# Performance work log

Measured on AMD Instinct MI355X. Metric: run time of the kernel, lower is better.

Reference implementation:

```python
import jax, jax.numpy as jnp
import numpy as np

H = 512          # HIDDEN_DIM
W = 480          # WINDOWWIDTH
NL = 8           # NUMLABELS (output_dim)
STEPS = W // 15  # 32 decoder steps
ATT = W // 16    # 30 attention positions
B = 4            # window batch
L = 12           # per-frame sequence length
D_IN = 32        # input_dim
N = B * W        # 1920 frame sequences


def _lstm(x, Wih, Whh, bih, bhh):
    # x: [T, Bn, Din] -> per-step hidden/cell states [T, Bn, Hd] (torch LSTM gate order i,f,g,o)
    xp = x @ Wih.T + (bih + bhh)
    h0 = jnp.zeros((x.shape[1], Whh.shape[1]), x.dtype)
    def step(carry, xt):
        h, c = carry
        g = xt + h @ Whh.T
        i, f, gg, o = jnp.split(g, 4, axis=-1)
        c = jax.nn.sigmoid(f) * c + jax.nn.sigmoid(i) * jnp.tanh(gg)
        h = jax.nn.sigmoid(o) * jnp.tanh(c)
        return (h, c), (h, c)
    _, (hs, cs) = jax.lax.scan(step, (h0, h0), xp)
    return hs, cs


def _bilstm(x, Wf, Uf, bf, cf, Wb, Ub, bb, cb):
    # x: [Bt, T, D] batch_first; returns ([Bt, T, 2H], h_fwd_final, h_bwd_final)
    xt = jnp.swapaxes(x, 0, 1)
    hf, _ = _lstm(xt, Wf, Uf, bf, cf)
    hb, _ = _lstm(xt[::-1], Wb, Ub, bb, cb)
    out = jnp.concatenate([hf, hb[::-1]], axis=-1)
    return jnp.swapaxes(out, 0, 1), hf[-1], hb[-1]


def _forward(xs, xlengths, enc_Wih, enc_Whh, enc_bih, enc_bhh,
             penc_Wih_f, penc_Whh_f, penc_bih_f, penc_bhh_f,
             penc_Wih_b, penc_Whh_b, penc_bih_b, penc_bhh_b,
             attn_W, attn_b, comb_W, comb_b,
             gru_Wih, gru_Whh, gru_bih, gru_bhh, out_W, out_b):
    # frame-level encoder: packed sequences -> (h, c) at each sequence's true length
    hs, cs = _lstm(xs, enc_Wih, enc_Whh, enc_bih, enc_bhh)   # [L, N, H] each
    idx = xlengths - 1
    ar = jnp.arange(N)
    ctx = jnp.concatenate([hs[idx, ar], cs[idx, ar]], axis=-1)  # [N, 2H]
    ctx = ctx.reshape(B, W // 2, 4 * H)
    # pyramidal BiLSTM stack (dropout is identity at eval)
    out = ctx
    hf = hb = None
    for i in range(4):
        out, hf, hb = _bilstm(ctx, penc_Wih_f[i], penc_Whh_f[i], penc_bih_f[i], penc_bhh_f[i],
                              penc_Wih_b[i], penc_Whh_b[i], penc_bih_b[i], penc_bhh_b[i])
        if i < 3:
            ctx = out.reshape(B, W // (2 ** (i + 2)), 4 * H)
    enc_out = out                                   # [B, ATT, 2H]
    hidden0 = jnp.concatenate([hf, hb], axis=-1)    # [B, 2H]

    def dstep(carry, _):
        inp, h = carry                              # [B, NL], [B, 2H]
        aw = jax.nn.softmax(jnp.concatenate([inp, h], axis=-1) @ attn_W.T + attn_b, axis=-1)
        ctxv = jnp.einsum('bt,btd->bd', aw, enc_out)
        x = jax.nn.relu(jnp.concatenate([inp, ctxv], axis=-1) @ comb_W.T + comb_b)
        # torch GRU cell (gate order r, z, n)
        gi = x @ gru_Wih.T + gru_bih
        gh = h @ gru_Whh.T + gru_bhh
        ir, iz, inn = jnp.split(gi, 3, axis=-1)
        hr, hz, hn = jnp.split(gh, 3, axis=-1)
        r = jax.nn.sigmoid(ir + hr)
        z = jax.nn.sigmoid(iz + hz)
        n = jnp.tanh(inn + r * hn)
        hnew = (1.0 - z) * n + z * h
        logp = jax.nn.log_softmax(hnew @ out_W.T + out_b, axis=-1)
        return (logp, hnew), logp                   # free-running: next input = log-probs

    inp0 = jnp.zeros((B, NL), xs.dtype)
    _, outs = jax.lax.scan(dstep, (inp0, hidden0), None, length=STEPS)  # [STEPS, B, NL]
    return jnp.swapaxes(outs, 0, 1).reshape(B * STEPS, NL)


def setup_inputs() -> dict:
    key = jax.random.key(0)
    ks = jax.random.split(key, 24)
    s = 0.03
    def nrm(k, shape):
        return jax.random.normal(k, shape, dtype=jnp.float32) * s
    return {
        'xs': jax.random.normal(ks[0], (L, N, D_IN), dtype=jnp.float32),
        'xlengths': jax.random.randint(ks[1], (N,), 1, L + 1, dtype=jnp.int32),
        'enc_Wih': nrm(ks[2], (4 * H, D_IN)),
        'enc_Whh': nrm(ks[3], (4 * H, H)),
        'enc_bih': nrm(ks[4], (4 * H,)),
        'enc_bhh': nrm(ks[5], (4 * H,)),
        'penc_Wih_f': nrm(ks[6], (4, 4 * H, 4 * H)),
        'penc_Whh_f': nrm(ks[7], (4, 4 * H, H)),
        'penc_bih_f': nrm(ks[8], (4, 4 * H)),
        'penc_bhh_f': nrm(ks[9], (4, 4 * H)),
        'penc_Wih_b': nrm(ks[10], (4, 4 * H, 4 * H)),
        'penc_Whh_b': nrm(ks[11], (4, 4 * H, H)),
        'penc_bih_b': nrm(ks[12], (4, 4 * H)),
        'penc_bhh_b': nrm(ks[13], (4, 4 * H)),
        'attn_W': nrm(ks[14], (ATT, 2 * H + NL)),
        'attn_b': nrm(ks[15], (ATT,)),
        'comb_W': nrm(ks[16], (H, 2 * H + NL)),
        'comb_b': nrm(ks[17], (H,)),
        'gru_Wih': nrm(ks[18], (3 * 2 * H, H)),
        'gru_Whh': nrm(ks[19], (3 * 2 * H, 2 * H)),
        'gru_bih': nrm(ks[20], (3 * 2 * H,)),
        'gru_bhh': nrm(ks[21], (3 * 2 * H,)),
        'out_W': nrm(ks[22], (NL, 2 * H)),
        'out_b': nrm(ks[23], (NL,)),
    }


def reference(xs, xlengths, enc_Wih, enc_Whh, enc_bih, enc_bhh,
              penc_Wih_f, penc_Whh_f, penc_bih_f, penc_bhh_f,
              penc_Wih_b, penc_Whh_b, penc_bih_b, penc_bhh_b,
              attn_W, attn_b, comb_W, comb_b,
              gru_Wih, gru_Whh, gru_bih, gru_bhh, out_W, out_b):
    return _forward(xs, xlengths, enc_Wih, enc_Whh, enc_bih, enc_bhh,
                    penc_Wih_f, penc_Whh_f, penc_bih_f, penc_bhh_f,
                    penc_Wih_b, penc_Whh_b, penc_bih_b, penc_bhh_b,
                    attn_W, attn_b, comb_W, comb_b,
                    gru_Wih, gru_Whh, gru_bih, gru_bhh, out_W, out_b)
```

## Files before the change

### kernel.cpp

```cpp
#include <hip/hip_runtime.h>
#include <stdint.h>

typedef __attribute__((ext_vector_type(8))) __bf16 bf16x8;
typedef __attribute__((ext_vector_type(4))) float f32x4;
typedef __attribute__((ext_vector_type(4))) unsigned u32x4;

#define DEVI static __device__ __forceinline__
#define SENT 0xFFFFFFFFu

DEVI bf16x8 bzero8(){ bf16x8 r;
#pragma unroll
  for (int i=0;i<8;++i) r[i]=(__bf16)0.0f; return r; }

DEVI bf16x8 ld8(const __bf16* p){ return *(const bf16x8*)p; }
DEVI void st8(__bf16* p, bf16x8 v){ *(bf16x8*)p = v; }

DEVI f32x4 MFMA(bf16x8 a, bf16x8 b, f32x4 c){
  return __builtin_amdgcn_mfma_f32_16x16x32_bf16(a, b, c, 0, 0, 0);
}

DEVI float sigf(float x){ return 1.0f/(1.0f+__expf(-x)); }

DEVI void ast(unsigned* p, unsigned v){ __hip_atomic_store(p, v, __ATOMIC_RELAXED, __HIP_MEMORY_SCOPE_AGENT); }

DEVI unsigned packbf(float a, float b){
  union { __bf16 h[2]; unsigned u; } x; x.h[0]=(__bf16)a; x.h[1]=(__bf16)b; return x.u;
}
DEVI float bflo(unsigned u){ return __builtin_bit_cast(float, u<<16); }
DEVI float bfhi(unsigned u){ return __builtin_bit_cast(float, u & 0xffff0000u); }

DEVI unsigned bad4(u32x4 v){ return (v[0]==SENT)|(v[1]==SENT)|(v[2]==SENT)|(v[3]==SENT); }

DEVI u32x4 ald4(const void* p){
  u32x4 v;
  asm volatile("global_load_dwordx4 %0, %1, off sc0 sc1\n\ts_waitcnt vmcnt(0)"
               : "=&v"(v) : "v"(p) : "memory");
  return v;
}
DEVI u32x4 poll4(const void* p){
  u32x4 v = ald4(p);
  while (bad4(v)){ __builtin_amdgcn_s_sleep(1); v = ald4(p); }
  return v;
}
DEVI void ald4x2(const void* p, u32x4& a, u32x4& b){
  asm volatile("global_load_dwordx4 %0, %2, off sc0 sc1\n\t"
               "global_load_dwordx4 %1, %2, off offset:16 sc0 sc1\n\t"
               "s_waitcnt vmcnt(0)"
               : "=&v"(a), "=&v"(b) : "v"(p) : "memory");
}
DEVI void poll4x2(const void* p, u32x4& a, u32x4& b){
  ald4x2(p, a, b);
  while (bad4(a) | bad4(b)){ __builtin_amdgcn_s_sleep(1); ald4x2(p, a, b); }
}

DEVI void packGroup(const float* W, int Nsrc, int Kreal, int NT, __bf16* dst, long g){
  int kt = (int)(g / (NT*64));
  int rem = (int)(g % (NT*64));
  int nt = rem >> 6, ln = rem & 63;
  int row = nt*16 + (ln & 15);
  int col = kt*32 + ((ln >> 4) << 3);
  bf16x8 v = bzero8();
  if (row < Nsrc){
#pragma unroll
    for (int j=0;j<8;++j){ int c = col + j; if (c < Kreal) v[j] = (__bf16)W[(long)row*Kreal + c]; }
  }
  st8(dst + g*8, v);
}

DEVI void packGroupCat(const float* Wih, const float* Whh, __bf16* dst, long g){
  int kt = (int)(g / (128*64));
  int rem = (int)(g % (128*64));
  int nt = rem >> 6, ln = rem & 63;
  int prow = nt*16 + (ln & 15);
  int src = (prow & 3)*512 + (prow >> 2);
  int col = kt*32 + ((ln >> 4) << 3);
  bf16x8 v;
  if (col < 32){
#pragma unroll
    for (int j=0;j<8;++j) v[j] = (__bf16)Wih[(long)src*32 + col + j];
  } else {
#pragma unroll
    for (int j=0;j<8;++j) v[j] = (__bf16)Whh[(long)src*512 + (col-32) + j];
  }
  st8(dst + g*8, v);
}

__global__ void initK(unsigned* hb){
  int g = blockIdx.x*256 + threadIdx.x;
  if (g < 6144) hb[2048 + g] = SENT;
}

__global__ void packSmallK(const float* __restrict__ xs, const float* __restrict__ eWih,
    const float* __restrict__ eWhh, const float* __restrict__ ebih, const float* __restrict__ ebhh,
    const float* __restrict__ attnW,
    __bf16* __restrict__ xsb, __bf16* __restrict__ wcatp, float* __restrict__ biasc,
    __bf16* __restrict__ attnp)
{
  long g = (long)blockIdx.x*blockDim.x + threadIdx.x;
  const long nWcat = 17L*128*64;
  const long nXs   = 92160;
  const long nBias = 2048;
  const long nAttn = 33L*2*64;
  if (g < nWcat){ packGroupCat(eWih, eWhh, wcatp, g); return; }
  g -= nWcat;
  if (g < nXs){
    const float* s = xs + g*8; bf16x8 v;
#pragma unroll
    for (int j=0;j<8;++j) v[j] = (__bf16)s[j];
    st8(xsb + g*8, v); return;
  }
  g -= nXs;
  if (g < nBias){ int src = ((int)g & 3)*512 + ((int)g >> 2); biasc[g] = ebih[src] + ebhh[src]; return; }
  g -= nBias;
  if (g < nAttn){ packGroup(attnW, 30, 1032, 2, attnp, g); return; }
}

__global__ void packPencK(const float* __restrict__ Wf, const float* __restrict__ Wb,
    const float* __restrict__ WhF, const float* __restrict__ WhB,
    const float* __restrict__ bihf, const float* __restrict__ bhhf,
    const float* __restrict__ bihb, const float* __restrict__ bhhb,
    __bf16* __restrict__ pf, __bf16* __restrict__ pb, float* __restrict__ bsum,
    __bf16* __restrict__ pwhh, unsigned* __restrict__ hpy)
{
  long g = (long)blockIdx.x*blockDim.x + threadIdx.x;
  const long nW = 64L*128*64;
  if (g < nW){ packGroup(Wf, 2048, 2048, 128, pf, g); return; }
  g -= nW;
  if (g < nW){ packGroup(Wb, 2048, 2048, 128, pb, g); return; }
  g -= nW;
  if (g < 2048){ bsum[g] = bihf[g] + bhhf[g]; return; }
  g -= 2048;
  if (g < 2048){ bsum[2048+g] = bihb[g] + bhhb[g]; return; }
  g -= 2048;
  if (g < 8192){
    hpy[g] = ((g >> 10) & 3) ? SENT : 0u;
    return;
  }
  g -= 8192;
  if (g < 262144){
    int lane = (int)(g & 63);
    int f    = (int)((g >> 6) & 31);
    int w    = (int)((g >> 11) & 3);
    int slot = (int)((g >> 13) & 15);
    int dir  = (int)((g >> 17) & 1);
    int kt = f >> 1, nt = f & 1;
    int row16 = lane & 15, kch = lane >> 4;
    int srow = w*512 + slot*32 + nt*16 + row16;
    int scol = kt*32 + kch*8;
    const float* W = dir ? WhB : WhF;
    bf16x8 v;
#pragma unroll
    for (int j=0;j<8;++j) v[j] = (__bf16)W[(long)srow*512 + scol + j];
    st8(pwhh + g*8, v);
  }
}

__global__ __launch_bounds__(256, 1) void encStepK(
    const __bf16* __restrict__ xsb,
    __bf16* __restrict__ henc,
    float* __restrict__ cenc,
    const __bf16* __restrict__ wcatp,
    const float* __restrict__ biasc,
    const int* __restrict__ xlen,
    __bf16* __restrict__ ctx,
    int t)
{
  __shared__ float glds[64][260];
  const int tid = threadIdx.x;
  const int w = tid >> 6, ln = tid & 63;
  const int m0 = blockIdx.x * 64;
  const int nb = blockIdx.y;
  f32x4 acc[16];
#pragma unroll
  for (int i=0;i<16;++i) acc[i] = (f32x4){0.f,0.f,0.f,0.f};

  const int arow = m0 + w*16 + (ln & 15);
  const int kc = (ln >> 4) << 3;
  const int ktEnd = (t == 0) ? 1 : 17;
  for (int kt = 0; kt < ktEnd; ++kt){
    bf16x8 a;
    if (kt == 0) a = ld8(xsb + ((long)t*1920 + arow)*32 + kc);
    else         a = ld8(henc + (long)arow*512 + (kt-1)*32 + kc);
    const __bf16* bp = wcatp + (((long)kt*128 + nb*16)*64 + ln)*8;
#pragma unroll
    for (int n2 = 0; n2 < 16; ++n2){
      bf16x8 b = ld8(bp + (long)n2*512);
      acc[n2] = MFMA(a, b, acc[n2]);
    }
  }
  const int r4 = (ln >> 4) << 2;
#pragma unroll
  for (int n2 = 0; n2 < 16; ++n2){
#pragma unroll
    for (int r = 0; r < 4; ++r)
      glds[w*16 + r4 + r][n2*16 + (ln & 15)] = acc[n2][r];
  }
  __syncthreads();
  for (int it = 0; it < 16; ++it){
    int idx = tid + it*256;
    int mrow = idx >> 6, hcl = idx & 63;
    int n = m0 + mrow;
    int hcg = nb*64 + hcl;
    float ig = glds[mrow][hcl*4+0] + biasc[nb*256 + hcl*4+0];
    float fg = glds[mrow][hcl*4+1] + biasc[nb*256 + hcl*4+1];
    float gg = glds[mrow][hcl*4+2] + biasc[nb*256 + hcl*4+2];
    float og = glds[mrow][hcl*4+3] + biasc[nb*256 + hcl*4+3];
    float c_old = (t == 0) ? 0.0f : cenc[(long)n*512 + hcg];
    float cn = sigf(fg)*c_old + sigf(ig)*tanhf(gg);
    float h  = sigf(og)*tanhf(cn);
    cenc[(long)n*512 + hcg] = cn;
    henc[(long)n*512 + hcg] = (__bf16)h;
    if (xlen[n] - 1 == t){
      ctx[(long)n*1024 + hcg]       = (__bf16)h;
      ctx[(long)n*1024 + 512 + hcg] = (__bf16)cn;
    }
  }
}

__global__ __launch_bounds__(1024) void pencInK(
   const __bf16* __restrict__ inb,
   const __bf16* __restrict__ wpf, const __bf16* __restrict__ wpb,
   const float* __restrict__ bsum,
   float* __restrict__ xpf, float* __restrict__ xpb,
   int M)
{
  const int tid = threadIdx.x, ln = tid & 63, wv = tid >> 6;
  const int rg = wv >> 2, cg = wv & 3;
  const int dir = blockIdx.z;
  const int m0 = blockIdx.x*64 + rg*16;
  const int nb = blockIdx.y;
  const __bf16* wp = dir ? wpb : wpf;
  float* xp = dir ? xpb : xpf;
  const float* bs = bsum + dir*2048;
  f32x4 acc[4];
#pragma unroll
  for (int i=0;i<4;++i) acc[i] = (f32x4){0.f,0.f,0.f,0.f};
  const int arow = m0 + (ln & 15);
  const int kc = (ln >> 4) << 3;
  const bool aok = arow < M;
  for (int kt = 0; kt < 64; ++kt){
    bf16x8 a = aok ? ld8(inb + (long)arow*2048 + kt*32 + kc) : bzero8();
    const __bf16* bp = wp + (((long)kt*128 + nb*16 + cg*4)*64 + ln)*8;
#pragma unroll
    for (int q = 0; q < 4; ++q){
      bf16x8 b = ld8(bp + (long)q*512);
      acc[q] = MFMA(a, b, acc[q]);
    }
  }
  const int r4 = (ln >> 4) << 2;
#pragma unroll
  for (int q = 0; q < 4; ++q){
    int col = (nb*16 + cg*4 + q)*16 + (ln & 15);
#pragma unroll
    for (int r = 0; r < 4; ++r){
      int rowo = m0 + r4 + r;
      if (rowo < M) xp[(long)rowo*2048 + col] = acc[q][r] + bs[col];
    }
  }
}

__global__ __launch_bounds__(256, 1) void pyrRecK(
  const __bf16* __restrict__ pwhh,
  const float* __restrict__ xpf, const float* __restrict__ xpb,
  __bf16* __restrict__ hbuf,
  __bf16* __restrict__ outb,
  float* __restrict__ outf,
  float* __restrict__ h0f, __bf16* __restrict__ h0b,
  int T, int isLast)
{
  __shared__ __align__(16) __bf16 hsL[2][4*512];
  __shared__ float glds[4][4][32];
  const int tid = threadIdx.x, ln = tid & 63, w = tid >> 6;
  const int bk = blockIdx.x;
  const int dir = bk >> 4, slot = bk & 15;
  const int hc0 = slot * 32;
  const float* xp = dir ? xpb : xpf;
  unsigned* hbu = (unsigned*)hbuf;

  bf16x8 BF[32];
  {
    const __bf16* wb = pwhh + ((((size_t)(dir*16 + slot)*4 + w)*32)*64 + ln)*8;
#pragma unroll
    for (int f = 0; f < 32; ++f) BF[f] = ld8(wb + (size_t)f*512);
  }

  const int arow = ln & 15;
  const int kc = (ln >> 4) << 3;
  float cv = 0.0f;
  float x0=0.f,x1=0.f,x2=0.f,x3=0.f;
  if (tid < 128){
    int pos0 = dir ? (T-1) : 0;
    const float* xr = xp + ((size_t)((tid>>5)*T + pos0))*2048 + hc0 + (tid & 31);
    x0 = xr[0]; x1 = xr[512]; x2 = xr[1024]; x3 = xr[1536];
  }

  for (int t = 0; t < T; ++t){
    int cur = t & 3, nxt = (t+1) & 3, clr = (t+2) & 3;
    int pos = dir ? (T-1-t) : t;
    {
      u32x4 v = poll4((const char*)hbuf + (size_t)(dir*4 + cur)*4096 + tid*16);
      ((u32x4*)hsL[t & 1])[tid] = v;
    }
    __syncthreads();
    if (tid < 64){
      int b = tid >> 4, i = tid & 15;
      ast(hbu + ((size_t)(dir*4 + clr)*4 + b)*256 + (hc0 >> 1) + i, SENT);
    }
    const __bf16* hs = hsL[t & 1];
    f32x4 a0 = {0.f,0.f,0.f,0.f}, a1 = a0, a2 = a0, a3 = a0;
#pragma unroll
    for (int kt = 0; kt < 16; kt += 2){
      bf16x8 aA = (arow < 4) ? ld8(hs + arow*512 + kt*32 + kc) : bzero8();
      bf16x8 aB = (arow < 4) ? ld8(hs + arow*512 + (kt+1)*32 + kc) : bzero8();
      a0 = MFMA(aA, BF[kt*2+0], a0);
      a1 = MFMA(aA, BF[kt*2+1], a1);
      a2 = MFMA(aB, BF[kt*2+2], a2);
      a3 = MFMA(aB, BF[kt*2+3], a3);
    }
    a0 += a2; a1 += a3;
    float xn0=0.f,xn1=0.f,xn2=0.f,xn3=0.f;
    if (t+1 < T && tid < 128){
      int pos2 = dir ? (T-2-t) : (t+1);
      const float* xr = xp + ((size_t)((tid>>5)*T + pos2))*2048 + hc0 + (tid & 31);
      xn0 = xr[0]; xn1 = xr[512]; xn2 = xr[1024]; xn3 = xr[1536];
    }
    if (ln < 16){
#pragma unroll
      for (int r=0;r<4;++r){ glds[w][r][ln] = a0[r]; glds[w][r][16+ln] = a1[r]; }
    }
    __syncthreads();
    if (tid < 128){
      int b = tid >> 5, hcl = tid & 31, hcg = hc0 + hcl;
      float ig = glds[0][b][hcl] + x0;
      float fg = glds[1][b][hcl] + x1;
      float gg = glds[2][b][hcl] + x2;
      float og = glds[3][b][hcl] + x3;
      cv = sigf(fg)*cv + sigf(ig)*tanhf(gg);
      float h = sigf(og)*tanhf(cv);
      float hn = __shfl_down(h, 1);
      if (!(hcl & 1))
        ast(hbu + ((size_t)(dir*4 + nxt)*4 + b)*256 + (hcg >> 1), packbf(h, hn));
      if (!isLast){
        outb[((long)(b*T + pos))*1024 + dir*512 + hcg] = (__bf16)h;
      } else {
        outf[((long)(b*T + pos))*1024 + dir*512 + hcg] = h;
        if (t == T-1){
          h0f[b*1024 + dir*512 + hcg] = h;
          h0b[b*1024 + dir*512 + hcg] = (__bf16)h;
        }
      }
    }
    x0=xn0; x1=xn1; x2=xn2; x3=xn3;
  }
}

__global__ __launch_bounds__(256) void precMK(const float* __restrict__ combW,
    const float* __restrict__ encOut, __bf16* __restrict__ Mb)
{
  __shared__ float eo[1024];
  int bt = blockIdx.x;
  int b = bt / 30, t = bt % 30;
  int tid = threadIdx.x;
  for (int i = tid; i < 1024; i += 256) eo[i] = encOut[((long)b*30 + t)*1024 + i];
  __syncthreads();
#pragma unroll 1
  for (int cc = 0; cc < 2; ++cc){
    int c = tid*2 + cc;
    const f32x4* wr4 = (const f32x4*)(combW + (long)c*1032 + 8);
    float s = 0.f;
    for (int d = 0; d < 256; ++d){
      f32x4 wv = wr4[d];
      s += wv[0]*eo[d*4] + wv[1]*eo[d*4+1] + wv[2]*eo[d*4+2] + wv[3]*eo[d*4+3];
    }
    Mb[((long)b*30 + t)*512 + c] = (__bf16)s;
  }
}

DEVI bf16x8 dfrag(const __bf16* base, const __bf16* inp, int row, int kt, int kc, int stride){
  if (row >= 4) return bzero8();
  int k = kt*32 + kc;
  if (k == 0) return ld8(inp + row*8);
  int off = k - 8;
  return (off < 1024) ? ld8(base + row*stride + off) : bzero8();
}

__global__ __launch_bounds__(256, 1) void decoderK(
  const float* __restrict__ gWih,
  const float* __restrict__ gWhh,
  const float* __restrict__ gbih, const float* __restrict__ gbhh,
  const float* __restrict__ combW,
  const float* __restrict__ combBias,
  const float* __restrict__ attnBias,
  const float* __restrict__ outW, const float* __restrict__ outBias,
  const __bf16* __restrict__ attnP,
  const __bf16* __restrict__ Mb,
  const float* __restrict__ h0f,
  __bf16* __restrict__ HB,
  float* __restrict__ dout)
{
  __shared__ __align__(16) __bf16 giL[96*512];
  __shared__ __align__(16) __bf16 outWL[8*1024];
  __shared__ __align__(16) __bf16 hL[4*1024];
  __shared__ __align__(16) __bf16 xL[4][520];
  __shared__ __align__(16) __bf16 WcIL[512][8];
  __shared__ __align__(16) __bf16 inpL[32];
  __shared__ float awL[4][32];
  __shared__ float redL[4][8];
  __shared__ float ghL[3][4][32];
  __shared__ float giO[3][4][32];
  __shared__ float biL[3][32], bhL[3][32];
  __shared__ float abL[30];
  __shared__ float cbAllL[512];

  const int tid = threadIdx.x, ln = tid & 63, w = tid >> 6;
  const int slot = blockIdx.x;
  const int hc0 = slot * 32;
  unsigned* HBu = (unsigned*)HB;

  for (int it = 0; it < 24; ++it){
    int g = it*256 + tid;
    int rho = g >> 6, c8 = g & 63;
    int gate = rho >> 5, r = rho & 31;
    const float* s = gWih + ((long)(gate*1024 + hc0 + r))*512 + c8*8;
    bf16x8 v;
#pragma unroll
    for (int j=0;j<8;++j) v[j] = (__bf16)s[j];
    st8((__bf16*)((char*)giL + ((rho*1024 + c8*16) ^ ((rho & 7) << 4))), v);
  }
  for (int it = 0; it < 32; ++it){
    int g = it*256 + tid;
    outWL[g] = (__bf16)outW[g];
  }
  for (int idx = tid; idx < 4096; idx += 256){
    int c = idx >> 3, j = idx & 7;
    WcIL[c][j] = (__bf16)combW[(long)c*1032 + j];
  }
  for (int idx = tid; idx < 512; idx += 256) cbAllL[idx] = combBias[idx];
  if (tid < 96){
    int g2 = tid >> 5, l = tid & 31;
    biL[g2][l] = gbih[g2*1024 + hc0 + l];
    bhL[g2][l] = gbhh[g2*1024 + hc0 + l];
  }
  if (tid < 30) abL[tid] = attnBias[tid];

  const int row = ln & 15, kc = (ln >> 4) << 3;
  bf16x8 bigF[66];
  if (w == 0){
#pragma unroll
    for (int nt = 0; nt < 2; ++nt)
#pragma unroll
      for (int kt = 0; kt < 33; ++kt)
        bigF[nt*33 + kt] = ld8(attnP + (((size_t)kt*2 + nt)*64 + ln)*8);
  } else {
    int gate = w - 1;
#pragma unroll
    for (int nt = 0; nt < 2; ++nt)
#pragma unroll
      for (int kt = 0; kt < 32; ++kt){
        const float* s = gWhh + ((long)(gate*1024 + hc0 + nt*16 + row))*1024 + kt*32 + kc;
        bf16x8 v;
#pragma unroll
        for (int j=0;j<8;++j) v[j] = (__bf16)s[j];
        bigF[nt*33 + kt] = v;
      }
  }

  float hold = 0.f;
  if (tid < 128) hold = h0f[(tid>>5)*1024 + hc0 + (tid & 31)];
  __syncthreads();

  for (int s = 0; s <= 32; ++s){
    int cur = s & 3, nxt = (s+1) & 3, clr = (s+2) & 3;
    {
      u32x4 q0, q1;
      poll4x2((const char*)HB + (size_t)cur*8192 + tid*32, q0, q1);
      ((u32x4*)hL)[tid*2]   = q0;
      ((u32x4*)hL)[tid*2+1] = q1;
    }
    __syncthreads();
    if (tid < 64){
      int b = tid >> 4, i = tid & 15;
      ast(HBu + ((size_t)clr*4 + b)*512 + (hc0 >> 1) + i, SENT);
    }
    if (s == 0){
      if (tid < 32) inpL[tid] = (__bf16)0.0f;
      __syncthreads();
    } else {
      int o = tid >> 3, sl = tid & 7;
      int b = o >> 3, l = o & 7;
      const unsigned* hlp = (const unsigned*)hL + b*512 + sl*64;
      const unsigned* wlp = (const unsigned*)outWL + l*512 + sl*64;
      float p = 0.f;
      for (int kk = 0; kk < 64; ++kk){
        unsigned u = hlp[kk], t2 = wlp[kk];
        p += bflo(u)*bflo(t2) + bfhi(u)*bfhi(t2);
      }
      p += __shfl_down(p, 4);
      p += __shfl_down(p, 2);
      p += __shfl_down(p, 1);
      if (sl == 0) redL[b][l] = p + outBias[l];
      __syncthreads();
      if (tid < 4){
        float m = redL[tid][0];
        for (int l2=1;l2<8;++l2) m = fmaxf(m, redL[tid][l2]);
        float sum = 0.f;
        for (int l2=0;l2<8;++l2) sum += __expf(redL[tid][l2]-m);
        float lse = m + __logf(sum);
        for (int l2=0;l2<8;++l2){
          float lp = redL[tid][l2] - lse;
          inpL[tid*8 + l2] = (__bf16)lp;
          if (slot == 0) dout[((long)tid*32 + (s-1))*8 + l2] = lp;
        }
      }
      __syncthreads();
    }
    if (s == 32) break;

    if (w == 0){
      f32x4 a0 = {0.f,0.f,0.f,0.f}, a1 = {0.f,0.f,0.f,0.f};
#pragma unroll
      for (int kt = 0; kt < 33; ++kt){
        bf16x8 a = dfrag(hL, inpL, row, kt, kc, 1024);
        a0 = MFMA(a, bigF[kt], a0);
        a1 = MFMA(a, bigF[33+kt], a1);
      }
      if (ln < 16){
#pragma unroll
        for (int r=0;r<4;++r) awL[r][ln] = a0[r] + abL[ln];
        if (16 + ln < 30){
#pragma unroll
          for (int r=0;r<4;++r) awL[r][16+ln] = a1[r] + abL[16+ln];
        }
      }
    } else {
      f32x4 a0 = {0.f,0.f,0.f,0.f}, a1 = {0.f,0.f,0.f,0.f};
#pragma unroll
      for (int kt = 0; kt < 32; ++kt){
        int k = kt*32 + kc;
        bf16x8 a = (row < 4) ? ld8(hL + row*1024 + k) : bzero8();
        a0 = MFMA(a, bigF[kt], a0);
        a1 = MFMA(a, bigF[33+kt], a1);
      }
      if (ln < 16){
        int gate = w - 1;
#pragma unroll
        for (int r=0;r<4;++r){
          ghL[gate][r][ln] = a0[r];
          ghL[gate][r][16+ln] = a1[r];
        }
      }
    }
    __syncthreads();
    if (tid < 4){
      float m = awL[tid][0];
      for (int t2=1;t2<30;++t2) m = fmaxf(m, awL[tid][t2]);
      float sum = 0.f;
      for (int t2=0;t2<30;++t2){ float e = __expf(awL[tid][t2]-m); awL[tid][t2] = e; sum += e; }
      float inv = 1.0f/sum;
      for (int t2=0;t2<30;++t2) awL[tid][t2] *= inv;
    }
    __syncthreads();
    {
      int c0 = tid*2;
#pragma unroll 1
      for (int b = 0; b < 4; ++b){
        float z0 = cbAllL[c0], z1 = cbAllL[c0+1];
#pragma unroll
        for (int j = 0; j < 8; ++j){
          float ij = (float)inpL[b*8 + j];
          z0 += (float)WcIL[c0][j]*ij;
          z1 += (float)WcIL[c0+1][j]*ij;
        }
        const unsigned* mp = (const unsigned*)Mb + (((long)b*30)*512 + c0)/2;
#pragma unroll
        for (int t2 = 0; t2 < 30; ++t2){
          unsigned u = mp[t2*256];
          float a = awL[b][t2];
          z0 += a*bflo(u);
          z1 += a*bfhi(u);
        }
        xL[b][c0]   = (__bf16)fmaxf(z0, 0.f);
        xL[b][c0+1] = (__bf16)fmaxf(z1, 0.f);
      }
    }
    __syncthreads();
    if (w >= 1){
      int gate = w - 1;
      f32x4 a0 = {0.f,0.f,0.f,0.f}, a1 = {0.f,0.f,0.f,0.f};
#pragma unroll
      for (int kt = 0; kt < 16; ++kt){
        int k = kt*32 + kc;
        bf16x8 a = (row < 4) ? ld8(&xL[row][k]) : bzero8();
        int r0 = gate*32 + row, r1 = r0 + 16;
        bf16x8 b0 = ld8((__bf16*)((char*)giL + ((r0*1024 + k*2) ^ ((r0 & 7) << 4))));
        bf16x8 b1 = ld8((__bf16*)((char*)giL + ((r1*1024 + k*2) ^ ((r1 & 7) << 4))));
        a0 = MFMA(a, b0, a0);
        a1 = MFMA(a, b1, a1);
      }
      if (ln < 16){
#pragma unroll
        for (int r=0;r<4;++r){
          giO[gate][r][ln] = a0[r] + biL[gate][ln];
          giO[gate][r][16+ln] = a1[r] + biL[gate][16+ln];
        }
      }
    }
    __syncthreads();
    if (tid < 128){
      int b = tid >> 5, l = tid & 31, hcg = hc0 + l;
      float rr = sigf(giO[0][b][l] + ghL[0][b][l] + bhL[0][l]);
      float zz = sigf(giO[1][b][l] + ghL[1][b][l] + bhL[1][l]);
      float nn = tanhf(giO[2][b][l] + rr*(ghL[2][b][l] + bhL[2][l]));
      float hnew = (1.0f - zz)*nn + zz*hold;
      hold = hnew;
      float h2 = __shfl_down(hnew, 1);
      if (!(l & 1))
        ast(HBu + ((size_t)nxt*4 + b)*512 + (hcg >> 1), packbf(hnew, h2));
    }
  }
}

static const size_t O_XSB   = 12288;
static const size_t O_WCATP = 1486848;
static const size_t O_BIASC = 3715072;
static const size_t O_HENC  = 3723264;
static const size_t O_PWHH  = 3723264;
static const size_t O_CENC  = 5689344;
static const size_t O_CTX   = 9621504;
static const size_t O_WIHPF = 13553664;
static const size_t O_WIHPB = 21942272;
static const size_t O_BSUM  = 30330880;
static const size_t O_XPF   = 30347264;
static const size_t O_XPB   = 38211584;
static const size_t O_HPYR  = 46075904;
static const size_t O_OUTA  = 46108672;
static const size_t O_OUTB  = 48074752;
static const size_t O_ENCO  = 49057792;
static const size_t O_H0F   = 49549312;
static const size_t O_HB    = 49565696;
static const size_t O_ATTNP = 49647616;
static const size_t O_M     = 49782784;

extern "C" void kernel_launch(void* const* d_in, const int* in_sizes, int n_in,
                              void* d_out, int out_size, void* d_ws, size_t ws_size,
                              hipStream_t stream)
{
  const float* xs    = (const float*)d_in[0];
  const int*   xlen  = (const int*)d_in[1];
  const float* eWih  = (const float*)d_in[2];
  const float* eWhh  = (const float*)d_in[3];
  const float* ebih  = (const float*)d_in[4];
  const float* ebhh  = (const float*)d_in[5];
  const float* pWihF = (const float*)d_in[6];
  const float* pWhhF = (const float*)d_in[7];
  const float* pbihF = (const float*)d_in[8];
  const float* pbhhF = (const float*)d_in[9];
  const float* pWihB = (const float*)d_in[10];
  const float* pWhhB = (const float*)d_in[11];
  const float* pbihB = (const float*)d_in[12];
  const float* pbhhB = (const float*)d_in[13];
  const float* attnW = (const float*)d_in[14];
  const float* attnb = (const float*)d_in[15];
  const float* combW = (const float*)d_in[16];
  const float* combb = (const float*)d_in[17];
  const float* gWih  = (const float*)d_in[18];
  const float* gWhh  = (const float*)d_in[19];
  const float* gbih  = (const float*)d_in[20];
  const float* gbhh  = (const float*)d_in[21];
  const float* outW  = (const float*)d_in[22];
  const float* outb  = (const float*)d_in[23];

  char* ws = (char*)d_ws;
  __bf16* XSB     = (__bf16*)(ws + O_XSB);
  __bf16* WCATP   = (__bf16*)(ws + O_WCATP);
  float*  BIASC   = (float*)(ws + O_BIASC);
  __bf16* HENC    = (__bf16*)(ws + O_HENC);
  __bf16* PWHH    = (__bf16*)(ws + O_PWHH);
  float*  CENC    = (float*)(ws + O_CENC);
  __bf16* CTX     = (__bf16*)(ws + O_CTX);
  __bf16* WIHPF   = (__bf16*)(ws + O_WIHPF);
  __bf16* WIHPB   = (__bf16*)(ws + O_WIHPB);
  float*  BSUM    = (float*)(ws + O_BSUM);
  float*  XPF     = (float*)(ws + O_XPF);
  float*  XPB     = (float*)(ws + O_XPB);
  __bf16* HPYR    = (__bf16*)(ws + O_HPYR);
  __bf16* OUTA    = (__bf16*)(ws + O_OUTA);
  __bf16* OUTB    = (__bf16*)(ws + O_OUTB);
  float*  ENCO    = (float*)(ws + O_ENCO);
  float*  H0F     = (float*)(ws + O_H0F);
  __bf16* HB      = (__bf16*)(ws + O_HB);
  __bf16* ATTNP   = (__bf16*)(ws + O_ATTNP);
  __bf16* MB      = (__bf16*)(ws + O_M);

  initK<<<24, 256, 0, stream>>>((unsigned*)HB);
  packSmallK<<<929, 256, 0, stream>>>(xs, eWih, eWhh, ebih, ebhh, attnW,
      XSB, WCATP, BIASC, ATTNP);

  for (int t = 0; t < 12; ++t)
    encStepK<<<dim3(30, 8), 256, 0, stream>>>(XSB, HENC, CENC, WCATP, BIASC, xlen, CTX, t);

  const int Ts[4] = {240, 120, 60, 30};
  const __bf16* ins[4] = {CTX, OUTA, OUTB, OUTA};
  __bf16* outs[4] = {OUTA, OUTB, OUTA, OUTB};
  for (int L = 0; L < 4; ++L){
    int T = Ts[L];
    packPencK<<<5168, 256, 0, stream>>>(pWihF + (long)L*2048*2048, pWihB + (long)L*2048*2048,
        pWhhF + (long)L*2048*512, pWhhB + (long)L*2048*512,
        pbihF + L*2048, pbhhF + L*2048, pbihB + L*2048, pbhhB + L*2048,
        WIHPF, WIHPB, BSUM, PWHH, (unsigned*)HPYR);
    int MBk = (4*T + 63)/64;
    pencInK<<<dim3(MBk, 8, 2), 1024, 0, stream>>>(ins[L], WIHPF, WIHPB, BSUM, XPF, XPB, 4*T);
    pyrRecK<<<32, 256, 0, stream>>>(PWHH, XPF, XPB, HPYR, outs[L], ENCO, H0F, HB,
        T, (L==3) ? 1 : 0);
  }

  precMK<<<120, 256, 0, stream>>>(combW, ENCO, MB);

  decoderK<<<32, 256, 0, stream>>>(gWih, gWhh, gbih, gbhh, combW, combb, attnb,
      outW, outb, ATTNP, MB, H0F, HB, (float*)d_out);
}
```

Before: 2.211 ms.

## Replace sentinel polling with monotonic per-block step flags in recurrent kernels

Inter-block synchronization in the pyramid recurrence and decoder kernels switches from polling hidden-state data for sentinel values (with clearing stores) to per-block monotonic step counters that are waited on, after which the state is read with double buffering instead of a 4-deep ring. The decoder's recurrent GRU weights are pre-packed to bf16 by a new kernel and streamed from global memory instead of being held in registers, and LDS arrays gain padding to reduce bank conflicts. The softmax also moves to a shuffle-based reduction. The aim is to cut polling traffic and register pressure, at the cost of an extra drain and barrier per step and extra global weight loads.

Result: slower. 2.816 ms (+27.4%).

```diff
diff --git a/kernel.cpp b/kernel.cpp
--- a/kernel.cpp
+++ b/kernel.cpp
@@ -6,7 +6,6 @@
 typedef __attribute__((ext_vector_type(4))) unsigned u32x4;
 
 #define DEVI static __device__ __forceinline__
-#define SENT 0xFFFFFFFFu
 
 DEVI bf16x8 bzero8(){ bf16x8 r;
 #pragma unroll
@@ -28,8 +27,6 @@
 }
 DEVI float bflo(unsigned u){ return __builtin_bit_cast(float, u<<16); }
 DEVI float bfhi(unsigned u){ return __builtin_bit_cast(float, u & 0xffff0000u); }
-
-DEVI unsigned bad4(u32x4 v){ return (v[0]==SENT)|(v[1]==SENT)|(v[2]==SENT)|(v[3]==SENT); }
 
 DEVI u32x4 ald4(const void* p){
   u32x4 v;
@@ -37,21 +34,25 @@
                : "=&v"(v) : "v"(p) : "memory");
   return v;
 }
-DEVI u32x4 poll4(const void* p){
-  u32x4 v = ald4(p);
-  while (bad4(v)){ __builtin_amdgcn_s_sleep(1); v = ald4(p); }
-  return v;
-}
 DEVI void ald4x2(const void* p, u32x4& a, u32x4& b){
   asm volatile("global_load_dwordx4 %0, %2, off sc0 sc1\n\t"
                "global_load_dwordx4 %1, %2, off offset:16 sc0 sc1\n\t"
                "s_waitcnt vmcnt(0)"
                : "=&v"(a), "=&v"(b) : "v"(p) : "memory");
 }
-DEVI void poll4x2(const void* p, u32x4& a, u32x4& b){
-  ald4x2(p, a, b);
-  while (bad4(a) | bad4(b)){ __builtin_amdgcn_s_sleep(1); ald4x2(p, a, b); }
-}
+
+DEVI void flagwait(const unsigned* flags, int n4, unsigned target){
+  int t = threadIdx.x;
+  if (t < n4){
+    const unsigned* p = flags + t*4;
+    for (;;){
+      u32x4 v = ald4(p);
+      if (v[0] >= target && v[1] >= target && v[2] >= target && v[3] >= target) break;
+      __builtin_amdgcn_s_sleep(1);
+    }
+  }
+}
+DEVI void drainvm(){ asm volatile("s_waitcnt vmcnt(0)" ::: "memory"); }
 
 DEVI void packGroup(const float* W, int Nsrc, int Kreal, int NT, __bf16* dst, long g){
   int kt = (int)(g / (NT*64));
@@ -85,9 +86,8 @@
   st8(dst + g*8, v);
 }
 
-__global__ void initK(unsigned* hb){
-  int g = blockIdx.x*256 + threadIdx.x;
-  if (g < 6144) hb[2048 + g] = SENT;
+__global__ void initK(unsigned* flg){
+  if (threadIdx.x < 64) flg[threadIdx.x] = 0u;
 }
 
 __global__ void packSmallK(const float* __restrict__ xs, const float* __restrict__ eWih,
@@ -120,7 +120,7 @@
     const float* __restrict__ bihf, const float* __restrict__ bhhf,
     const float* __restrict__ bihb, const float* __restrict__ bhhb,
     __bf16* __restrict__ pf, __bf16* __restrict__ pb, float* __restrict__ bsum,
-    __bf16* __restrict__ pwhh, unsigned* __restrict__ hpy)
+    __bf16* __restrict__ pwhh, unsigned* __restrict__ flg)
 {
   long g = (long)blockIdx.x*blockDim.x + threadIdx.x;
   const long nW = 64L*128*64;
@@ -132,11 +132,8 @@
   g -= 2048;
   if (g < 2048){ bsum[2048+g] = bihb[g] + bhhb[g]; return; }
   g -= 2048;
-  if (g < 8192){
-    hpy[g] = ((g >> 10) & 3) ? SENT : 0u;
-    return;
-  }
-  g -= 8192;
+  if (g < 32){ flg[g] = 0u; return; }
+  g -= 32;
   if (g < 262144){
     int lane = (int)(g & 63);
     int f    = (int)((g >> 6) & 31);
@@ -153,6 +150,23 @@
     for (int j=0;j<8;++j) v[j] = (__bf16)W[(long)srow*512 + scol + j];
     st8(pwhh + g*8, v);
   }
+}
+
+__global__ void packDecK(const float* __restrict__ gWhh, __bf16* __restrict__ pgh)
+{
+  long g = (long)blockIdx.x*256 + threadIdx.x;
+  const long nGH = 32L*3*2*32*64;
+  if (g >= nGH) return;
+  int lane = (int)(g & 63); long idx = g >> 6;
+  int kt = (int)(idx & 31); int nt = (int)((idx >> 5) & 1);
+  int sg = (int)(idx >> 6);
+  int gate = sg % 3, slot = sg / 3;
+  int r = gate*1024 + slot*32 + nt*16 + (lane & 15);
+  int c = kt*32 + ((lane >> 4) << 3);
+  bf16x8 v;
+#pragma unroll
+  for (int j=0;j<8;++j) v[j] = (__bf16)gWhh[(long)r*1024 + c + j];
+  st8(pgh + g*8, v);
 }
 
 __global__ __launch_bounds__(256, 1) void encStepK(
@@ -266,9 +280,10 @@
   __bf16* __restrict__ outb,
   float* __restrict__ outf,
   float* __restrict__ h0f, __bf16* __restrict__ h0b,
+  unsigned* __restrict__ flg,
   int T, int isLast)
 {
-  __shared__ __align__(16) __bf16 hsL[2][4*512];
+  __shared__ __align__(16) __bf16 hsL[2][4*528];
   __shared__ float glds[4][4][32];
   const int tid = threadIdx.x, ln = tid & 63, w = tid >> 6;
   const int bk = blockIdx.x;
@@ -276,6 +291,7 @@
   const int hc0 = slot * 32;
   const float* xp = dir ? xpb : xpf;
   unsigned* hbu = (unsigned*)hbuf;
+  unsigned* myflg = flg + dir*16;
 
   bf16x8 BF[32];
   {
@@ -283,6 +299,7 @@
 #pragma unroll
     for (int f = 0; f < 32; ++f) BF[f] = ld8(wb + (size_t)f*512);
   }
+  for (int i = tid; i < 1056; i += 256) ((unsigned*)hsL[0])[i] = 0u;
 
   const int arow = ln & 15;
   const int kc = (ln >> 4) << 3;
@@ -293,25 +310,24 @@
     const float* xr = xp + ((size_t)((tid>>5)*T + pos0))*2048 + hc0 + (tid & 31);
     x0 = xr[0]; x1 = xr[512]; x2 = xr[1024]; x3 = xr[1536];
   }
+  __syncthreads();
 
   for (int t = 0; t < T; ++t){
-    int cur = t & 3, nxt = (t+1) & 3, clr = (t+2) & 3;
     int pos = dir ? (T-1-t) : t;
-    {
-      u32x4 v = poll4((const char*)hbuf + (size_t)(dir*4 + cur)*4096 + tid*16);
-      ((u32x4*)hsL[t & 1])[tid] = v;
-    }
-    __syncthreads();
-    if (tid < 64){
-      int b = tid >> 4, i = tid & 15;
-      ast(hbu + ((size_t)(dir*4 + clr)*4 + b)*256 + (hc0 >> 1) + i, SENT);
-    }
+    if (t > 0){
+      flagwait(myflg, 4, (unsigned)t);
+      __syncthreads();
+      u32x4 v = ald4((const char*)hbuf + (size_t)(dir*2 + (t&1))*4096 + tid*16);
+      int e0 = tid*8, r = e0 >> 9, o = e0 & 511;
+      *(u32x4*)(hsL[t&1] + r*528 + o) = v;
+    }
+    __syncthreads();
     const __bf16* hs = hsL[t & 1];
     f32x4 a0 = {0.f,0.f,0.f,0.f}, a1 = a0, a2 = a0, a3 = a0;
 #pragma unroll
     for (int kt = 0; kt < 16; kt += 2){
-      bf16x8 aA = (arow < 4) ? ld8(hs + arow*512 + kt*32 + kc) : bzero8();
-      bf16x8 aB = (arow < 4) ? ld8(hs + arow*512 + (kt+1)*32 + kc) : bzero8();
+      bf16x8 aA = (arow < 4) ? ld8(hs + arow*528 + kt*32 + kc) : bzero8();
+      bf16x8 aB = (arow < 4) ? ld8(hs + arow*528 + (kt+1)*32 + kc) : bzero8();
       a0 = MFMA(aA, BF[kt*2+0], a0);
       a1 = MFMA(aA, BF[kt*2+1], a1);
       a2 = MFMA(aB, BF[kt*2+2], a2);
@@ -339,7 +355,7 @@
       float h = sigf(og)*tanhf(cv);
       float hn = __shfl_down(h, 1);
       if (!(hcl & 1))
-        ast(hbu + ((size_t)(dir*4 + nxt)*4 + b)*256 + (hcg >> 1), packbf(h, hn));
+        ast(hbu + ((size_t)(dir*2 + ((t+1)&1))*4 + b)*256 + (hcg >> 1), packbf(h, hn));
       if (!isLast){
         outb[((long)(b*T + pos))*1024 + dir*512 + hcg] = (__bf16)h;
       } else {
@@ -350,7 +366,9 @@
         }
       }
     }
-    x0=xn0; x1=xn1; x2=xn2; x3=xn3;
+    drainvm();
+    __syncthreads();
+    if (tid == 0) ast(myflg + slot, (unsigned)(t+1));
   }
 }
 
@@ -386,23 +404,25 @@
 
 __global__ __launch_bounds__(256, 1) void decoderK(
   const float* __restrict__ gWih,
-  const float* __restrict__ gWhh,
   const float* __restrict__ gbih, const float* __restrict__ gbhh,
   const float* __restrict__ combW,
   const float* __restrict__ combBias,
   const float* __restrict__ attnBias,
   const float* __restrict__ outW, const float* __restrict__ outBias,
   const __bf16* __restrict__ attnP,
+  const __bf16* __restrict__ pgh,
   const __bf16* __restrict__ Mb,
   const float* __restrict__ h0f,
+  const __bf16* __restrict__ h0b,
   __bf16* __restrict__ HB,
+  unsigned* __restrict__ flg,
   float* __restrict__ dout)
 {
   __shared__ __align__(16) __bf16 giL[96*512];
-  __shared__ __align__(16) __bf16 outWL[8*1024];
-  __shared__ __align__(16) __bf16 hL[4*1024];
-  __shared__ __align__(16) __bf16 xL[4][520];
-  __shared__ __align__(16) __bf16 WcIL[512][8];
+  __shared__ __align__(16) __bf16 outWL[8*1040];
+  __shared__ __align__(16) __bf16 hL[4*1040];
+  __shared__ __align__(16) __bf16 xL[4][528];
+  __shared__ __align__(16) __bf16 WcIT[8][520];
   __shared__ __align__(16) __bf16 inpL[32];
   __shared__ float awL[4][32];
   __shared__ float redL[4][8];
@@ -429,11 +449,12 @@
   }
   for (int it = 0; it < 32; ++it){
     int g = it*256 + tid;
-    outWL[g] = (__bf16)outW[g];
+    int r = g >> 10, c = g & 1023;
+    outWL[r*1040 + c] = (__bf16)outW[g];
   }
   for (int idx = tid; idx < 4096; idx += 256){
     int c = idx >> 3, j = idx & 7;
-    WcIL[c][j] = (__bf16)combW[(long)c*1032 + j];
+    WcIT[j][c] = (__bf16)combW[(long)c*1032 + j];
   }
   for (int idx = tid; idx < 512; idx += 256) cbAllL[idx] = combBias[idx];
   if (tid < 96){
@@ -444,55 +465,35 @@
   if (tid < 30) abL[tid] = attnBias[tid];
 
   const int row = ln & 15, kc = (ln >> 4) << 3;
-  bf16x8 bigF[66];
-  if (w == 0){
-#pragma unroll
-    for (int nt = 0; nt < 2; ++nt)
-#pragma unroll
-      for (int kt = 0; kt < 33; ++kt)
-        bigF[nt*33 + kt] = ld8(attnP + (((size_t)kt*2 + nt)*64 + ln)*8);
-  } else {
-    int gate = w - 1;
-#pragma unroll
-    for (int nt = 0; nt < 2; ++nt)
-#pragma unroll
-      for (int kt = 0; kt < 32; ++kt){
-        const float* s = gWhh + ((long)(gate*1024 + hc0 + nt*16 + row))*1024 + kt*32 + kc;
-        bf16x8 v;
-#pragma unroll
-        for (int j=0;j<8;++j) v[j] = (__bf16)s[j];
-        bigF[nt*33 + kt] = v;
-      }
-  }
-
   float hold = 0.f;
   if (tid < 128) hold = h0f[(tid>>5)*1024 + hc0 + (tid & 31)];
   __syncthreads();
 
   for (int s = 0; s <= 32; ++s){
-    int cur = s & 3, nxt = (s+1) & 3, clr = (s+2) & 3;
+    if (s > 0) flagwait(flg, 8, (unsigned)s);
+    __syncthreads();
     {
+      const char* src = (s == 0) ? (const char*)h0b
+                                 : ((const char*)HB + (size_t)(s&1)*8192);
       u32x4 q0, q1;
-      poll4x2((const char*)HB + (size_t)cur*8192 + tid*32, q0, q1);
-      ((u32x4*)hL)[tid*2]   = q0;
-      ((u32x4*)hL)[tid*2+1] = q1;
-    }
-    __syncthreads();
-    if (tid < 64){
-      int b = tid >> 4, i = tid & 15;
-      ast(HBu + ((size_t)clr*4 + b)*512 + (hc0 >> 1) + i, SENT);
-    }
+      ald4x2(src + tid*32, q0, q1);
+      int e0 = tid*16, r0 = e0 >> 10, o0 = e0 & 1023;
+      u32x4* d = (u32x4*)(hL + r0*1040 + o0);
+      d[0] = q0; d[1] = q1;
+    }
+    __syncthreads();
     if (s == 0){
       if (tid < 32) inpL[tid] = (__bf16)0.0f;
       __syncthreads();
     } else {
       int o = tid >> 3, sl = tid & 7;
       int b = o >> 3, l = o & 7;
-      const unsigned* hlp = (const unsigned*)hL + b*512 + sl*64;
-      const unsigned* wlp = (const unsigned*)outWL + l*512 + sl*64;
+      const unsigned* hrow = (const unsigned*)hL + b*520;
+      const unsigned* wrow = (const unsigned*)outWL + l*520;
       float p = 0.f;
-      for (int kk = 0; kk < 64; ++kk){
-        unsigned u = hlp[kk], t2 = wlp[kk];
+#pragma unroll 8
+      for (int j = 0; j < 64; ++j){
+        unsigned u = hrow[sl + 8*j], t2 = wrow[sl + 8*j];
         p += bflo(u)*bflo(t2) + bfhi(u)*bfhi(t2);
       }
       p += __shfl_down(p, 4);
@@ -520,9 +521,11 @@
       f32x4 a0 = {0.f,0.f,0.f,0.f}, a1 = {0.f,0.f,0.f,0.f};
 #pragma unroll
       for (int kt = 0; kt < 33; ++kt){
-        bf16x8 a = dfrag(hL, inpL, row, kt, kc, 1024);
-        a0 = MFMA(a, bigF[kt], a0);
-        a1 = MFMA(a, bigF[33+kt], a1);
+        bf16x8 a = dfrag(hL, inpL, row, kt, kc, 1040);
+        bf16x8 b0 = ld8(attnP + (((size_t)kt*2 + 0)*64 + ln)*8);
+        bf16x8 b1 = ld8(attnP + (((size_t)kt*2 + 1)*64 + ln)*8);
+        a0 = MFMA(a, b0, a0);
+        a1 = MFMA(a, b1, a1);
       }
       if (ln < 16){
 #pragma unroll
@@ -533,31 +536,37 @@
         }
       }
     } else {
-      f32x4 a0 = {0.f,0.f,0.f,0.f}, a1 = {0.f,0.f,0.f,0.f};
+      int gate = w - 1;
+      const __bf16* bp = pgh + (((size_t)(slot*3 + gate)*64)*64 + ln)*8;
+      f32x4 g0 = {0.f,0.f,0.f,0.f}, g1 = g0;
 #pragma unroll
       for (int kt = 0; kt < 32; ++kt){
         int k = kt*32 + kc;
-        bf16x8 a = (row < 4) ? ld8(hL + row*1024 + k) : bzero8();
-        a0 = MFMA(a, bigF[kt], a0);
-        a1 = MFMA(a, bigF[33+kt], a1);
+        bf16x8 a = (row < 4) ? ld8(hL + row*1040 + k) : bzero8();
+        g0 = MFMA(a, ld8(bp + (size_t)kt*512), g0);
+        g1 = MFMA(a, ld8(bp + (size_t)(32+kt)*512), g1);
       }
       if (ln < 16){
-        int gate = w - 1;
-#pragma unroll
-        for (int r=0;r<4;++r){
-          ghL[gate][r][ln] = a0[r];
-          ghL[gate][r][16+ln] = a1[r];
-        }
-      }
-    }
-    __syncthreads();
-    if (tid < 4){
-      float m = awL[tid][0];
-      for (int t2=1;t2<30;++t2) m = fmaxf(m, awL[tid][t2]);
-      float sum = 0.f;
-      for (int t2=0;t2<30;++t2){ float e = __expf(awL[tid][t2]-m); awL[tid][t2] = e; sum += e; }
-      float inv = 1.0f/sum;
-      for (int t2=0;t2<30;++t2) awL[tid][t2] *= inv;
+#pragma unroll
+        for (int r=0;r<4;++r){ ghL[gate][r][ln] = g0[r]; ghL[gate][r][16+ln] = g1[r]; }
+      }
+    }
+    __syncthreads();
+    if (tid < 64){
+      int b = tid >> 4, l16 = tid & 15;
+      float v0 = awL[b][l16];
+      float v1 = (l16+16 < 30) ? awL[b][l16+16] : -1e30f;
+      float m = fmaxf(v0, v1);
+#pragma unroll
+      for (int d=1; d<16; d<<=1) m = fmaxf(m, __shfl_xor(m, d));
+      float e0 = __expf(v0 - m);
+      float e1 = (l16+16 < 30) ? __expf(v1 - m) : 0.f;
+      float sum = e0 + e1;
+#pragma unroll
+      for (int d=1; d<16; d<<=1) sum += __shfl_xor(sum, d);
+      float inv = 1.0f / sum;
+      awL[b][l16] = e0 * inv;
+      awL[b][l16+16] = e1 * inv;
     }
     __syncthreads();
     {
@@ -568,8 +577,8 @@
 #pragma unroll
         for (int j = 0; j < 8; ++j){
           float ij = (float)inpL[b*8 + j];
-          z0 += (float)WcIL[c0][j]*ij;
-          z1 += (float)WcIL[c0+1][j]*ij;
+          z0 += (float)WcIT[j][c0]*ij;
+          z1 += (float)WcIT[j][c0+1]*ij;
         }
         const unsigned* mp = (const unsigned*)Mb + (((long)b*30)*512 + c0)/2;
 #pragma unroll
@@ -615,11 +624,15 @@
       hold = hnew;
       float h2 = __shfl_down(hnew, 1);
       if (!(l & 1))
-        ast(HBu + ((size_t)nxt*4 + b)*512 + (hcg >> 1), packbf(hnew, h2));
-    }
-  }
-}
-
+        ast(HBu + ((size_t)((s+1)&1)*4 + b)*512 + (hcg >> 1), packbf(hnew, h2));
+    }
+    drainvm();
+    __syncthreads();
+    if (tid == 0) ast(flg + slot, (unsigned)(s+1));
+  }
+}
+
+static const size_t O_FLG   = 0;
 static const size_t O_XSB   = 12288;
 static const size_t O_WCATP = 1486848;
 static const size_t O_BIASC = 3715072;
@@ -628,6 +641,7 @@
 static const size_t O_CENC  = 5689344;
 static const size_t O_CTX   = 9621504;
 static const size_t O_WIHPF = 13553664;
+static const size_t O_PGH   = 13553664;
 static const size_t O_WIHPB = 21942272;
 static const size_t O_BSUM  = 30330880;
 static const size_t O_XPF   = 30347264;
@@ -638,6 +652,7 @@
 static const size_t O_ENCO  = 49057792;
 static const size_t O_H0F   = 49549312;
 static const size_t O_HB    = 49565696;
+static const size_t O_H0B   = 49581824;
 static const size_t O_ATTNP = 49647616;
 static const size_t O_M     = 49782784;
 
@@ -671,6 +686,7 @@
   const float* outb  = (const float*)d_in[23];
 
   char* ws = (char*)d_ws;
+  unsigned* FLG   = (unsigned*)(ws + O_FLG);
   __bf16* XSB     = (__bf16*)(ws + O_XSB);
   __bf16* WCATP   = (__bf16*)(ws + O_WCATP);
   float*  BIASC   = (float*)(ws + O_BIASC);
@@ -680,6 +696,7 @@
   __bf16* CTX     = (__bf16*)(ws + O_CTX);
   __bf16* WIHPF   = (__bf16*)(ws + O_WIHPF);
   __bf16* WIHPB   = (__bf16*)(ws + O_WIHPB);
+  __bf16* PGH     = (__bf16*)(ws + O_PGH);
   float*  BSUM    = (float*)(ws + O_BSUM);
   float*  XPF     = (float*)(ws + O_XPF);
   float*  XPB     = (float*)(ws + O_XPB);
@@ -689,10 +706,11 @@
   float*  ENCO    = (float*)(ws + O_ENCO);
   float*  H0F     = (float*)(ws + O_H0F);
   __bf16* HB      = (__bf16*)(ws + O_HB);
+  __bf16* H0B     = (__bf16*)(ws + O_H0B);
   __bf16* ATTNP   = (__bf16*)(ws + O_ATTNP);
   __bf16* MB      = (__bf16*)(ws + O_M);
 
-  initK<<<24, 256, 0, stream>>>((unsigned*)HB);
+  initK<<<1, 256, 0, stream>>>(FLG);
   packSmallK<<<929, 256, 0, stream>>>(xs, eWih, eWhh, ebih, ebhh, attnW,
       XSB, WCATP, BIASC, ATTNP);
 
@@ -704,18 +722,20 @@
   __bf16* outs[4] = {OUTA, OUTB, OUTA, OUTB};
   for (int L = 0; L < 4; ++L){
     int T = Ts[L];
-    packPencK<<<5168, 256, 0, stream>>>(pWihF + (long)L*2048*2048, pWihB + (long)L*2048*2048,
+    packPencK<<<5137, 256, 0, stream>>>(pWihF + (long)L*2048*2048, pWihB + (long)L*2048*2048,
         pWhhF + (long)L*2048*512, pWhhB + (long)L*2048*512,
         pbihF + L*2048, pbhhF + L*2048, pbihB + L*2048, pbhhB + L*2048,
-        WIHPF, WIHPB, BSUM, PWHH, (unsigned*)HPYR);
+        WIHPF, WIHPB, BSUM, PWHH, FLG);
     int MBk = (4*T + 63)/64;
     pencInK<<<dim3(MBk, 8, 2), 1024, 0, stream>>>(ins[L], WIHPF, WIHPB, BSUM, XPF, XPB, 4*T);
-    pyrRecK<<<32, 256, 0, stream>>>(PWHH, XPF, XPB, HPYR, outs[L], ENCO, H0F, HB,
-        T, (L==3) ? 1 : 0);
+    if (L == 3)
+      packDecK<<<1536, 256, 0, stream>>>(gWhh, PGH);
+    pyrRecK<<<32, 256, 0, stream>>>(PWHH, XPF, XPB, HPYR, outs[L], ENCO, H0F, H0B,
+        FLG, T, (L==3) ? 1 : 0);
   }
 
   precMK<<<120, 256, 0, stream>>>(combW, ENCO, MB);
 
-  decoderK<<<32, 256, 0, stream>>>(gWih, gWhh, gbih, gbhh, combW, combb, attnb,
-      outW, outb, ATTNP, MB, H0F, HB, (float*)d_out);
-}
+  decoderK<<<32, 256, 0, stream>>>(gWih, gbih, gbhh, combW, combb, attnb, outW, outb,
+      ATTNP, PGH, MB, H0F, H0B, HB, FLG + 32, (float*)d_out);
+}
```
